# Kernel optimization log

Measured on AMD Instinct MI355X. Metric: run time of the kernel, lower is better.

## Reference

```python
import jax, jax.numpy as jnp
import numpy as np

B, K, M, D = 8, 4096, 4096, 512
L = K + M  # output length along axis -2
MASK_INIT_STD = 0.01  # jax.nn.initializers.normal() default stddev


def setup_inputs() -> dict:
    key = jax.random.key(0)
    k1, k2, k3 = jax.random.split(key, 3)
    inputs = jax.random.normal(k1, (B, K, D), dtype=jnp.float32)
    mask_embedding = jax.random.normal(k2, (D,), dtype=jnp.float32) * MASK_INIT_STD
    # Per-batch permutations of [0, L) so keep/fill indices partition the output.
    perm = jax.vmap(lambda k: jax.random.permutation(k, L))(jax.random.split(k3, B))
    keep_position_ids = perm[:, :K].astype(jnp.int32)
    mask_position_ids = perm[:, K:].astype(jnp.int32)
    return {
        "inputs": inputs,
        "mask_position_ids": mask_position_ids,
        "keep_position_ids": keep_position_ids,
        "mask_embedding": mask_embedding,
        "axis": -2,
    }


def reference(inputs, mask_position_ids, keep_position_ids, mask_embedding, axis):
    # Faithful math of MaskFiller with keep_position_ids given (fill_by_scatter):
    # out[b, keep_ids[b, k], :] = inputs[b, k, :]
    # out[b, mask_ids[b, m], :] = mask_embedding
    # The original implements this as one-hot dot_generals; a true scatter is the
    # same math without the O(L*K) blow-up.
    assert axis == -2
    b, k, d = inputs.shape
    m = mask_position_ids.shape[-1]
    length = k + m
    bidx = jnp.arange(b)[:, None]
    out = jnp.zeros((b, length, d), dtype=inputs.dtype)
    out = out.at[bidx, keep_position_ids].set(inputs)
    upd = jnp.broadcast_to(mask_embedding.astype(inputs.dtype), (b, m, d))
    out = out.at[bidx, mask_position_ids].set(upd)
    return out
```

## Files before the change

kernel.cpp:

```cpp
#include <hip/hip_runtime.h>
#include <hip/hip_bf16.h>


constexpr int B = 8;
constexpr int K = 4096;
constexpr int M = 4096;
constexpr int L = K + M;
constexpr int D = 512;
constexpr int D4 = D / 4;

__global__ __launch_bounds__(128)
void MaskFiller_scatter_kernel(const float4* __restrict__ inputs,
                               const int* __restrict__ mask_ids,
                               const int* __restrict__ keep_ids,
                               const float4* __restrict__ emb,
                               float4* __restrict__ out) {
    const int row = blockIdx.x;
    const int b   = row / L;
    const int r   = row - b * L;
    const int d4  = threadIdx.x;

    float4 v;
    int dst;
    if (r < K) {
        dst = keep_ids[b * K + r];
        v   = inputs[(size_t)(b * K + r) * D4 + d4];
    } else {
        const int m = r - K;
        dst = mask_ids[b * M + m];
        v   = emb[d4];
    }
    out[((size_t)b * L + dst) * D4 + d4] = v;
}

extern "C" void kernel_launch(void* const* d_in, const int* in_sizes, int n_in,
                              void* d_out, int out_size, void* d_ws, size_t ws_size,
                              hipStream_t stream) {
    const float4* inputs   = (const float4*)d_in[0];
    const int*    mask_ids = (const int*)d_in[1];
    const int*    keep_ids = (const int*)d_in[2];
    const float4* emb      = (const float4*)d_in[3];
    float4* out = (float4*)d_out;

    dim3 grid(B * L);
    dim3 block(128);
    MaskFiller_scatter_kernel<<<grid, block, 0, stream>>>(inputs, mask_ids, keep_ids, emb, out);
}
```

Measured before the change: 185.7 us.

## Use persistent grid-stride scatter with nontemporal loads and stores

```diff
diff --git a/kernel.cpp b/kernel.cpp
--- a/kernel.cpp
+++ b/kernel.cpp
@@ -2,47 +2,59 @@
 #include <hip/hip_bf16.h>
 
 
-constexpr int B = 8;
-constexpr int K = 4096;
-constexpr int M = 4096;
-constexpr int L = K + M;
-constexpr int D = 512;
+typedef float f4 __attribute__((ext_vector_type(4)));
+
+constexpr int B  = 8;
+constexpr int K  = 4096;
+constexpr int M  = 4096;
+constexpr int L  = K + M;
+constexpr int D  = 512;
 constexpr int D4 = D / 4;
 
-__global__ __launch_bounds__(128)
-void MaskFiller_scatter_kernel(const float4* __restrict__ inputs,
+constexpr int THREADS = 256;
+constexpr int ROWS_PER_ITER = THREADS / D4;
+constexpr int GRID = 2048;
+
+__global__ __launch_bounds__(THREADS)
+void MaskFiller_scatter_kernel(const f4* __restrict__ inputs,
                                const int* __restrict__ mask_ids,
                                const int* __restrict__ keep_ids,
-                               const float4* __restrict__ emb,
-                               float4* __restrict__ out) {
-    const int row = blockIdx.x;
-    const int b   = row / L;
-    const int r   = row - b * L;
-    const int d4  = threadIdx.x;
+                               const f4* __restrict__ emb,
+                               f4* __restrict__ out) {
+    const int d4  = threadIdx.x & (D4 - 1);
+    const int sub = threadIdx.x >> 7;
+    const f4 ev = emb[d4];
 
-    float4 v;
-    int dst;
-    if (r < K) {
-        dst = keep_ids[b * K + r];
-        v   = inputs[(size_t)(b * K + r) * D4 + d4];
-    } else {
-        const int m = r - K;
-        dst = mask_ids[b * M + m];
-        v   = emb[d4];
+    const int stride = GRID * ROWS_PER_ITER;
+    int row = blockIdx.x * ROWS_PER_ITER + sub;
+
+    #pragma unroll 4
+    for (; row < B * L; row += stride) {
+        const int b = row >> 13;
+        const int r = row & (L - 1);
+        int dst;
+        f4 v;
+        if (r < K) {
+            const int src = (b << 12) + r;
+            dst = keep_ids[src];
+            v   = __builtin_nontemporal_load(&inputs[((size_t)src << 7) + d4]);
+        } else {
+            dst = mask_ids[(b << 12) + (r - K)];
+            v   = ev;
+        }
+        __builtin_nontemporal_store(v, &out[(((size_t)(b << 13) + dst) << 7) + d4]);
     }
-    out[((size_t)b * L + dst) * D4 + d4] = v;
 }
 
 extern "C" void kernel_launch(void* const* d_in, const int* in_sizes, int n_in,
                               void* d_out, int out_size, void* d_ws, size_t ws_size,
                               hipStream_t stream) {
-    const float4* inputs   = (const float4*)d_in[0];
-    const int*    mask_ids = (const int*)d_in[1];
-    const int*    keep_ids = (const int*)d_in[2];
-    const float4* emb      = (const float4*)d_in[3];
-    float4* out = (float4*)d_out;
+    const f4*  inputs   = (const f4*)d_in[0];
+    const int* mask_ids = (const int*)d_in[1];
+    const int* keep_ids = (const int*)d_in[2];
+    const f4*  emb      = (const f4*)d_in[3];
+    f4* out = (f4*)d_out;
 
-    dim3 grid(B * L);
-    dim3 block(128);
-    MaskFiller_scatter_kernel<<<grid, block, 0, stream>>>(inputs, mask_ids, keep_ids, emb, out);
+    MaskFiller_scatter_kernel<<<dim3(GRID), dim3(THREADS), 0, stream>>>(
+        inputs, mask_ids, keep_ids, emb, out);
 }
```

Result: no change. 186.8 us (+0.6%).
